# Performance work log

Hardware: AMD Instinct MI355X
Metric: run time of the kernel (lower is better)

## Reference

```python
import jax, jax.numpy as jnp
import numpy as np

N_M = 100000  # musicians
N_T = 100000  # tracks
E = 400000
D = 128


def _sage(x_src, x_dst, edge, W_l, b_l, W_r, n_dst):
    """PyG SAGEConv: lin_l(mean_{j in N(i)} x_src[j]) + lin_r(x_dst[i])."""
    src, dst = edge[0], edge[1]
    msg = x_src[src]                                   # [E, D] gather
    agg = jax.ops.segment_sum(msg, dst, num_segments=n_dst)
    cnt = jax.ops.segment_sum(jnp.ones((edge.shape[1],), x_src.dtype), dst,
                              num_segments=n_dst)
    agg = agg / jnp.maximum(cnt, 1.0)[:, None]         # mean aggregation
    return agg @ W_l.T + b_l + x_dst @ W_r.T


def setup_inputs() -> dict:
    key = jax.random.key(0)
    ks = jax.random.split(key, 7)
    scale = 0.05
    return {
        "x_m": jax.random.normal(ks[0], (N_M, D), jnp.float32),
        "x_t": jax.random.normal(ks[1], (N_T, D), jnp.float32),
        "Wl": jax.random.normal(ks[2], (3, 2, D, D), jnp.float32) * scale,
        "bl": jnp.zeros((3, 2, D), jnp.float32),
        "Wr": jax.random.normal(ks[3], (3, 2, D, D), jnp.float32) * scale,
        "edge_mt": jax.random.randint(ks[4], (2, E), 0, N_T, jnp.int32).astype(jnp.int64),
        "edge_tm": jax.random.randint(ks[5], (2, E), 0, N_M, jnp.int32).astype(jnp.int64),
    }


def reference(x_m, x_t, Wl, bl, Wr, edge_mt, edge_tm):
    # 3 HeteroConv(SAGEConv) layers; dropout=0.0 is identity.
    for layer in range(3):
        # edge type 0: musician -plays_on-> track  (dst = track)
        new_t = _sage(x_m, x_t, edge_mt, Wl[layer, 0], bl[layer, 0], Wr[layer, 0], N_T)
        # edge type 1: track -features-> musician  (dst = musician)
        new_m = _sage(x_t, x_m, edge_tm, Wl[layer, 1], bl[layer, 1], Wr[layer, 1], N_M)
        if layer < 2:
            new_m = jax.nn.relu(new_m)
            new_t = jax.nn.relu(new_t)
        x_m, x_t = new_m, new_t
    return x_m, x_t
```

## Files before the change

kernel.cpp:

```cpp
#include <hip/hip_runtime.h>
#include <hip/hip_bf16.h>

typedef __bf16 bf16_t;
typedef __attribute__((ext_vector_type(4))) __bf16 bf16x4;
typedef __attribute__((ext_vector_type(8))) __bf16 bf16x8;
typedef __attribute__((ext_vector_type(4))) float f32x4;

#define DIM 128
#define GTILE 32

__device__ __forceinline__ void gl_lds16(const void* g, void* l) {
    __builtin_amdgcn_global_load_lds(
        (const __attribute__((address_space(1))) unsigned int*)g,
        (__attribute__((address_space(3))) unsigned int*)l, 16, 0, 0);
}

__global__ void prep_count(const float* __restrict__ Wl, const float* __restrict__ Wr,
                           bf16_t* __restrict__ Wc,
                           const int* __restrict__ dA, int* __restrict__ cA,
                           const int* __restrict__ dB, int* __restrict__ cB, int E,
                           const float* __restrict__ xm, bf16_t* __restrict__ xbm, int CM,
                           const float* __restrict__ xt, bf16_t* __restrict__ xbt, int CT,
                           int PB, int CB) {
    int blk = blockIdx.x;
    if (blk < PB) {
        int idx = blk * 256 + threadIdx.x;
        if (idx >= 6 * 128 * 256) return;
        int k = idx & 255;
        int n = (idx >> 8) & 127;
        int s = idx >> 15;
        float v;
        if (k < 128) v = Wl[((size_t)s * 128 + n) * 128 + k];
        else         v = Wr[((size_t)s * 128 + n) * 128 + (k - 128)];
        Wc[idx] = (bf16_t)v;
    } else if (blk < PB + CB) {
        int i = (blk - PB) * 256 + threadIdx.x;
        if (i < E) atomicAdd(&cA[dA[i]], 1);
        else if (i < 2 * E) atomicAdd(&cB[dB[i - E]], 1);
    } else {
        int i = (blk - PB - CB) * 256 + threadIdx.x;
        const float* src; bf16_t* dst;
        if (i < CM) { src = xm; dst = xbm; }
        else if ((i -= CM) < CT) { src = xt; dst = xbt; }
        else return;
        float4 a = ((const float4*)src)[(size_t)i * 2];
        float4 b = ((const float4*)src)[(size_t)i * 2 + 1];
        bf16x8 r;
        r[0] = (bf16_t)a.x; r[1] = (bf16_t)a.y; r[2] = (bf16_t)a.z; r[3] = (bf16_t)a.w;
        r[4] = (bf16_t)b.x; r[5] = (bf16_t)b.y; r[6] = (bf16_t)b.z; r[7] = (bf16_t)b.w;
        *(bf16x8*)(dst + (size_t)i * 8) = r;
    }
}

__global__ __launch_bounds__(256) void scan_local2(
    const int* __restrict__ cntA, int* __restrict__ partA, int* __restrict__ bsumA,
    int MA, int NBA,
    const int* __restrict__ cntB, int* __restrict__ partB, int* __restrict__ bsumB,
    int MB) {
    int blk = blockIdx.x;
    const int* cnt; int* partial; int* blocksum; int M; int b;
    if (blk < NBA) { cnt = cntA; partial = partA; blocksum = bsumA; M = MA; b = blk; }
    else           { cnt = cntB; partial = partB; blocksum = bsumB; M = MB; b = blk - NBA; }
    __shared__ int sdata[256];
    int i = b * 256 + threadIdx.x;
    int v = (i < M) ? cnt[i] : 0;
    sdata[threadIdx.x] = v;
    __syncthreads();
    for (int off = 1; off < 256; off <<= 1) {
        int t = (threadIdx.x >= off) ? sdata[threadIdx.x - off] : 0;
        __syncthreads();
        sdata[threadIdx.x] += t;
        __syncthreads();
    }
    int incl = sdata[threadIdx.x];
    if (i < M) partial[i] = incl - v;
    if (threadIdx.x == 255) blocksum[b] = incl;
}

__global__ __launch_bounds__(256) void scan_blocks2(int* __restrict__ bsA, int NA,
                                                    int* __restrict__ bsB, int NBcnt) {
    int* blocksum = blockIdx.x ? bsB : bsA;
    int NB = blockIdx.x ? NBcnt : NA;
    __shared__ int sdata[256];
    __shared__ int running;
    if (threadIdx.x == 0) running = 0;
    __syncthreads();
    for (int base = 0; base < NB; base += 256) {
        int i = base + threadIdx.x;
        int v = (i < NB) ? blocksum[i] : 0;
        sdata[threadIdx.x] = v;
        __syncthreads();
        for (int off = 1; off < 256; off <<= 1) {
            int t = (threadIdx.x >= off) ? sdata[threadIdx.x - off] : 0;
            __syncthreads();
            sdata[threadIdx.x] += t;
            __syncthreads();
        }
        int incl = sdata[threadIdx.x];
        int r = running;
        __syncthreads();
        if (i < NB) blocksum[i] = incl - v + r;
        if (threadIdx.x == 0) running = r + sdata[255];
        __syncthreads();
    }
}

__global__ __launch_bounds__(256) void add_offsets2(
    const int* __restrict__ pA, const int* __restrict__ bsA,
    int* __restrict__ rsA, int* __restrict__ curA, int MA, int NBA,
    const int* __restrict__ pB, const int* __restrict__ bsB,
    int* __restrict__ rsB, int* __restrict__ curB, int MB) {
    int blk = blockIdx.x;
    const int *partial, *blocksum; int *rowstart, *cursor; int M, b;
    if (blk < NBA) { partial = pA; blocksum = bsA; rowstart = rsA; cursor = curA; M = MA; b = blk; }
    else           { partial = pB; blocksum = bsB; rowstart = rsB; cursor = curB; M = MB; b = blk - NBA; }
    int i = b * 256 + threadIdx.x;
    if (i < M) {
        int rs = partial[i] + blocksum[i >> 8];
        rowstart[i] = rs;
        cursor[i] = rs;
    }
}

__global__ void bin_edges2(const int* __restrict__ sA, const int* __restrict__ dA,
                           int* __restrict__ curA, int* __restrict__ csrA,
                           const int* __restrict__ sB, const int* __restrict__ dB,
                           int* __restrict__ curB, int* __restrict__ csrB, int E) {
    int e = blockIdx.x * blockDim.x + threadIdx.x;
    if (e < E) {
        int d = dA[e];
        int pos = atomicAdd(&curA[d], 1);
        csrA[pos] = sA[e];
    } else if (e < 2 * E) {
        int i = e - E;
        int d = dB[i];
        int pos = atomicAdd(&curB[d], 1);
        csrB[pos] = sB[i];
    }
}

#define A0SZ 8192
#define A1SZ 8192

template <int MODE>
__global__ __launch_bounds__(256, 3) void fused2(
    const bf16_t* __restrict__ gsA, const int* __restrict__ rsA,
    const int* __restrict__ cnA, const int* __restrict__ csA,
    const bf16_t* __restrict__ a1A, const bf16_t* __restrict__ WcA,
    const float* __restrict__ bA, void* __restrict__ oA, int Ma,
    const bf16_t* __restrict__ gsB, const int* __restrict__ rsB,
    const int* __restrict__ cnB, const int* __restrict__ csB,
    const bf16_t* __restrict__ a1B, const bf16_t* __restrict__ WcB,
    const float* __restrict__ bB, void* __restrict__ oB, int Mb) {
    __shared__ char smem[A0SZ + 2 * A1SZ];

    const int tid  = threadIdx.x;
    const int wid  = tid >> 6;
    const int lane = tid & 63;
    const int quad = lane >> 4;
    const int l16  = lane & 15;

    const int side = blockIdx.x & 1;
    const int t0   = blockIdx.x >> 1;
    const int gs   = gridDim.x >> 1;

    const bf16_t *gsrc, *a1p; const int *rsx, *cnx, *csx;
    const bf16_t* Wc; const float* bias; void* outp; int M;
    if (side == 0) { gsrc = gsA; rsx = rsA; cnx = cnA; csx = csA; a1p = a1A;
                     Wc = WcA; bias = bA; outp = oA; M = Ma; }
    else           { gsrc = gsB; rsx = rsB; cnx = cnB; csx = csB; a1p = a1B;
                     Wc = WcB; bias = bB; outp = oB; M = Mb; }
    const int nt = (M + GTILE - 1) / GTILE;
    if (t0 >= nt) return;

    bf16x8 breg[2][8];
#pragma unroll
    for (int ct = 0; ct < 2; ++ct)
#pragma unroll
        for (int kt = 0; kt < 8; ++kt)
            breg[ct][kt] = *(const bf16x8*)(
                Wc + (size_t)(wid * 32 + ct * 16 + l16) * 256 + kt * 32 + quad * 8);

    const float bcol0 = bias[wid * 32 + l16];
    const float bcol1 = bias[wid * 32 + 16 + l16];
    const int sw = l16 & 7;

    int s_row[2], s_off[2];
#pragma unroll
    for (int c = 0; c < 2; ++c) {
        int o = wid * 2048 + c * 1024 + lane * 16;
        int row = o >> 8;
        int ch  = (o >> 4) & 15;
        s_row[c] = row;
        s_off[c] = (ch ^ (row & 7)) * 8;
    }

    auto STAGE = [&](int b, int t) {
        const int r0 = t * GTILE;
        char* base = smem + A0SZ + b * A1SZ;
#pragma unroll
        for (int c = 0; c < 2; ++c) {
            int grow = r0 + s_row[c]; if (grow >= M) grow = M - 1;
            gl_lds16(a1p + (size_t)grow * DIM + s_off[c],
                     base + wid * 2048 + c * 1024);
        }
    };

    auto GATHER = [&](int t) {
        const int hw  = tid >> 5;
        const int l32 = tid & 31;
        char* a0 = smem;
#pragma unroll 1
        for (int rr = 0; rr < 4; ++rr) {
            int r = hw * 4 + rr;
            int d = t * GTILE + r;
            float4 acc0 = {0.f, 0.f, 0.f, 0.f};
            float4 acc1 = {0.f, 0.f, 0.f, 0.f};
            int n = 0;
            if (d < M) {
                int start = rsx[d];
                n = cnx[d];
                for (int k = 0; k < n; k += 8) {
                    int sv[8];
#pragma unroll
                    for (int j = 0; j < 8; ++j)
                        sv[j] = csx[start + min(k + j, n - 1)];
                    float4 vv[8];
#pragma unroll
                    for (int j = 0; j < 8; ++j) {
                        bf16x4 b4 = *(const bf16x4*)(gsrc + (size_t)sv[j] * DIM + l32 * 4);
                        vv[j] = (float4){(float)b4[0], (float)b4[1],
                                         (float)b4[2], (float)b4[3]};
                    }
#pragma unroll
                    for (int j = 0; j < 8; j += 2) {
                        float w0 = (k + j     < n) ? 1.f : 0.f;
                        float w1 = (k + j + 1 < n) ? 1.f : 0.f;
                        acc0.x += vv[j].x * w0; acc0.y += vv[j].y * w0;
                        acc0.z += vv[j].z * w0; acc0.w += vv[j].w * w0;
                        acc1.x += vv[j + 1].x * w1; acc1.y += vv[j + 1].y * w1;
                        acc1.z += vv[j + 1].z * w1; acc1.w += vv[j + 1].w * w1;
                    }
                }
            }
            float invn = 1.0f / (float)max(n, 1);
            bf16x4 res;
            res[0] = (bf16_t)((acc0.x + acc1.x) * invn);
            res[1] = (bf16_t)((acc0.y + acc1.y) * invn);
            res[2] = (bf16_t)((acc0.z + acc1.z) * invn);
            res[3] = (bf16_t)((acc0.w + acc1.w) * invn);
            *(bf16x4*)(a0 + r * 256 + (((l32 >> 1) ^ (r & 7)) << 4) + ((l32 & 1) << 3)) = res;
        }
    };

    auto COMPUTE = [&](int b, int t) {
        const int r0 = t * GTILE;
        const char* a0base = smem;
        const char* a1base = smem + A0SZ + b * A1SZ;
        f32x4 acc[2][2];
#pragma unroll
        for (int rt = 0; rt < 2; ++rt) {
            acc[rt][0] = (f32x4){0.f, 0.f, 0.f, 0.f};
            acc[rt][1] = (f32x4){0.f, 0.f, 0.f, 0.f};
        }
#pragma unroll
        for (int rt = 0; rt < 2; ++rt) {
            const int row = rt * 16 + l16;
            bf16x8 alo[4];
#pragma unroll
            for (int kt = 0; kt < 4; ++kt)
                alo[kt] = *(const bf16x8*)(a0base + row * 256 + ((kt * 4 + quad) ^ sw) * 16);
#pragma unroll
            for (int kt = 0; kt < 4; ++kt) {
                acc[rt][0] = __builtin_amdgcn_mfma_f32_16x16x32_bf16(alo[kt], breg[0][kt], acc[rt][0], 0, 0, 0);
                acc[rt][1] = __builtin_amdgcn_mfma_f32_16x16x32_bf16(alo[kt], breg[1][kt], acc[rt][1], 0, 0, 0);
            }
#pragma unroll
            for (int kt = 0; kt < 4; ++kt) {
                bf16x8 ah = *(const bf16x8*)(a1base + row * 256 + ((kt * 4 + quad) ^ sw) * 16);
                acc[rt][0] = __builtin_amdgcn_mfma_f32_16x16x32_bf16(ah, breg[0][kt + 4], acc[rt][0], 0, 0, 0);
                acc[rt][1] = __builtin_amdgcn_mfma_f32_16x16x32_bf16(ah, breg[1][kt + 4], acc[rt][1], 0, 0, 0);
            }
        }
#pragma unroll
        for (int ct = 0; ct < 2; ++ct) {
            const int col = wid * 32 + ct * 16 + l16;
            const float bv = ct ? bcol1 : bcol0;
#pragma unroll
            for (int rt = 0; rt < 2; ++rt)
#pragma unroll
                for (int r = 0; r < 4; ++r) {
                    int row = r0 + rt * 16 + quad * 4 + r;
                    if (row < M) {
                        float v = acc[rt][ct][r] + bv;
                        if (MODE == 1) v = fmaxf(v, 0.f);
                        if constexpr (MODE == 2)
                            ((float*)outp)[(size_t)row * DIM + col] = v;
                        else
                            ((bf16_t*)outp)[(size_t)row * DIM + col] = (bf16_t)v;
                    }
                }
        }
    };

    STAGE(0, t0);
    int cur = 0;
    for (int t = t0; t < nt; t += gs, cur ^= 1) {
        const int nxt = t + gs;
        if (nxt < nt) STAGE(cur ^ 1, nxt);
        GATHER(t);
        __syncthreads();
        COMPUTE(cur, t);
        __syncthreads();
    }
}

extern "C" void kernel_launch(void* const* d_in, const int* in_sizes, int n_in,
                              void* d_out, int out_size, void* d_ws, size_t ws_size,
                              hipStream_t stream) {
    const float* x_m = (const float*)d_in[0];
    const float* x_t = (const float*)d_in[1];
    const float* Wl  = (const float*)d_in[2];
    const float* bl  = (const float*)d_in[3];
    const float* Wr  = (const float*)d_in[4];
    const int* e_mt  = (const int*)d_in[5];
    const int* e_tm  = (const int*)d_in[6];

    const int Mm = in_sizes[0] / DIM;
    const int Mt = in_sizes[1] / DIM;
    const int E  = in_sizes[5] / 2;
    const int NBt = (Mt + 255) / 256;
    const int NBm = (Mm + 255) / 256;

    float* out_m = (float*)d_out;
    float* out_t = (float*)d_out + (size_t)Mm * DIM;

    char* ws = (char*)d_ws;
    size_t off = 0;
    auto alloc = [&](size_t bytes) -> void* {
        void* p = ws + off;
        off += (bytes + 255) & ~(size_t)255;
        return p;
    };
    bf16_t* xbm    = (bf16_t*)alloc((size_t)Mm * DIM * 2);
    bf16_t* xbt    = (bf16_t*)alloc((size_t)Mt * DIM * 2);
    bf16_t* xb_m0  = (bf16_t*)alloc((size_t)Mm * DIM * 2);
    bf16_t* xb_t0  = (bf16_t*)alloc((size_t)Mt * DIM * 2);
    bf16_t* xb_m1  = (bf16_t*)alloc((size_t)Mm * DIM * 2);
    bf16_t* xb_t1  = (bf16_t*)alloc((size_t)Mt * DIM * 2);
    int*    cnt_t  = (int*)alloc((size_t)Mt * 4);
    int*    cnt_m  = (int*)alloc((size_t)Mm * 4);
    int*    rs_t   = (int*)alloc((size_t)Mt * 4);
    int*    rs_m   = (int*)alloc((size_t)Mm * 4);
    int*    cur_tb = (int*)alloc((size_t)Mt * 4);
    int*    cur_mb = (int*)alloc((size_t)Mm * 4);
    int*    part_t = (int*)alloc((size_t)Mt * 4);
    int*    part_m = (int*)alloc((size_t)Mm * 4);
    int*    bsum_t = (int*)alloc((size_t)NBt * 4);
    int*    bsum_m = (int*)alloc((size_t)NBm * 4);
    int*    csr_t  = (int*)alloc((size_t)E * 4);
    int*    csr_m  = (int*)alloc((size_t)E * 4);
    bf16_t* Wc     = (bf16_t*)alloc((size_t)6 * 128 * 256 * 2);

    hipMemsetAsync(cnt_t, 0, (size_t)Mt * 4, stream);
    hipMemsetAsync(cnt_m, 0, (size_t)Mm * 4, stream);

    const int CM = Mm * DIM / 8, CT = Mt * DIM / 8;
    const int PB = (6 * 128 * 256 + 255) / 256;
    const int CB = (2 * E + 255) / 256;
    const int XB = (CM + CT + 255) / 256;
    prep_count<<<PB + CB + XB, 256, 0, stream>>>(Wl, Wr, Wc,
                                                 e_mt + E, cnt_t, e_tm + E, cnt_m, E,
                                                 x_m, xbm, CM, x_t, xbt, CT, PB, CB);

    scan_local2<<<NBt + NBm, 256, 0, stream>>>(cnt_t, part_t, bsum_t, Mt, NBt,
                                               cnt_m, part_m, bsum_m, Mm);
    scan_blocks2<<<2, 256, 0, stream>>>(bsum_t, NBt, bsum_m, NBm);
    add_offsets2<<<NBt + NBm, 256, 0, stream>>>(part_t, bsum_t, rs_t, cur_tb, Mt, NBt,
                                                part_m, bsum_m, rs_m, cur_mb, Mm);
    bin_edges2<<<(2 * E + 255) / 256, 256, 0, stream>>>(e_mt, e_mt + E, cur_tb, csr_t,
                                                        e_tm, e_tm + E, cur_mb, csr_m, E);

    int GG = 1536;
    {
        int ntT = (Mt + GTILE - 1) / GTILE, ntM = (Mm + GTILE - 1) / GTILE;
        int need = 2 * ((ntT > ntM) ? ntT : ntM);
        if (GG > need) GG = need;
        GG &= ~1;
        if (GG < 2) GG = 2;
    }

    const float* biasT0 = bl + 0 * DIM;  const float* biasM0 = bl + 1 * DIM;
    const float* biasT1 = bl + 2 * DIM;  const float* biasM1 = bl + 3 * DIM;
    const float* biasT2 = bl + 4 * DIM;  const float* biasM2 = bl + 5 * DIM;
    const bf16_t* WcT0 = Wc + 0 * 128 * 256;  const bf16_t* WcM0 = Wc + 1 * 128 * 256;
    const bf16_t* WcT1 = Wc + 2 * 128 * 256;  const bf16_t* WcM1 = Wc + 3 * 128 * 256;
    const bf16_t* WcT2 = Wc + 4 * 128 * 256;  const bf16_t* WcM2 = Wc + 5 * 128 * 256;

    fused2<1><<<GG, 256, 0, stream>>>(
        xbm, rs_t, cnt_t, csr_t, xbt, WcT0, biasT0, xb_t0, Mt,
        xbt, rs_m, cnt_m, csr_m, xbm, WcM0, biasM0, xb_m0, Mm);
    fused2<1><<<GG, 256, 0, stream>>>(
        xb_m0, rs_t, cnt_t, csr_t, xb_t0, WcT1, biasT1, xb_t1, Mt,
        xb_t0, rs_m, cnt_m, csr_m, xb_m0, WcM1, biasM1, xb_m1, Mm);
    fused2<2><<<GG, 256, 0, stream>>>(
        xb_m1, rs_t, cnt_t, csr_t, xb_t1, WcT2, biasT2, out_t, Mt,
        xb_t1, rs_m, cnt_m, csr_m, xb_m1, WcM2, biasM2, out_m, Mm);
}
```

Before: 527.5 us.

## Merge three-kernel scan into one wave-shuffle scan and interleave two-row gathers

Replaces the three-pass prefix scan (local scan, block-sum scan, add offsets) with a single kernel of two 1024-thread blocks. Each block walks its whole count array using wave shuffles and writes a trailing rowstart entry, so degree is now taken as rs[d+1]-rs[d] and the separate count array is no longer read in the fused layers. The neighbor-mean gather now handles two destination rows at once with 4-wide unrolled loads, keeping more independent memory requests in flight. The trade-offs are a serial scan run by only two blocks, and wasted clamped loads when the two interleaved rows have different degrees.

```diff
diff --git a/kernel.cpp b/kernel.cpp
--- a/kernel.cpp
+++ b/kernel.cpp
@@ -52,74 +52,48 @@
     }
 }
 
-__global__ __launch_bounds__(256) void scan_local2(
-    const int* __restrict__ cntA, int* __restrict__ partA, int* __restrict__ bsumA,
-    int MA, int NBA,
-    const int* __restrict__ cntB, int* __restrict__ partB, int* __restrict__ bsumB,
-    int MB) {
-    int blk = blockIdx.x;
-    const int* cnt; int* partial; int* blocksum; int M; int b;
-    if (blk < NBA) { cnt = cntA; partial = partA; blocksum = bsumA; M = MA; b = blk; }
-    else           { cnt = cntB; partial = partB; blocksum = bsumB; M = MB; b = blk - NBA; }
-    __shared__ int sdata[256];
-    int i = b * 256 + threadIdx.x;
-    int v = (i < M) ? cnt[i] : 0;
-    sdata[threadIdx.x] = v;
+__global__ __launch_bounds__(1024) void scan_all(
+    const int* __restrict__ cntA, int* __restrict__ rsA, int* __restrict__ curA, int MA,
+    const int* __restrict__ cntB, int* __restrict__ rsB, int* __restrict__ curB, int MB) {
+    const int* cnt; int* rs; int* cur; int M;
+    if (blockIdx.x == 0) { cnt = cntA; rs = rsA; cur = curA; M = MA; }
+    else                 { cnt = cntB; rs = rsB; cur = curB; M = MB; }
+    __shared__ int swv[16];
+    __shared__ int srun;
+    const int tid  = threadIdx.x;
+    const int wave = tid >> 6;
+    const int lane = tid & 63;
+    if (tid == 0) srun = 0;
     __syncthreads();
-    for (int off = 1; off < 256; off <<= 1) {
-        int t = (threadIdx.x >= off) ? sdata[threadIdx.x - off] : 0;
-        __syncthreads();
-        sdata[threadIdx.x] += t;
-        __syncthreads();
-    }
-    int incl = sdata[threadIdx.x];
-    if (i < M) partial[i] = incl - v;
-    if (threadIdx.x == 255) blocksum[b] = incl;
-}
-
-__global__ __launch_bounds__(256) void scan_blocks2(int* __restrict__ bsA, int NA,
-                                                    int* __restrict__ bsB, int NBcnt) {
-    int* blocksum = blockIdx.x ? bsB : bsA;
-    int NB = blockIdx.x ? NBcnt : NA;
-    __shared__ int sdata[256];
-    __shared__ int running;
-    if (threadIdx.x == 0) running = 0;
-    __syncthreads();
-    for (int base = 0; base < NB; base += 256) {
-        int i = base + threadIdx.x;
-        int v = (i < NB) ? blocksum[i] : 0;
-        sdata[threadIdx.x] = v;
-        __syncthreads();
-        for (int off = 1; off < 256; off <<= 1) {
-            int t = (threadIdx.x >= off) ? sdata[threadIdx.x - off] : 0;
-            __syncthreads();
-            sdata[threadIdx.x] += t;
-            __syncthreads();
-        }
-        int incl = sdata[threadIdx.x];
-        int r = running;
-        __syncthreads();
-        if (i < NB) blocksum[i] = incl - v + r;
-        if (threadIdx.x == 0) running = r + sdata[255];
-        __syncthreads();
-    }
-}
-
-__global__ __launch_bounds__(256) void add_offsets2(
-    const int* __restrict__ pA, const int* __restrict__ bsA,
-    int* __restrict__ rsA, int* __restrict__ curA, int MA, int NBA,
-    const int* __restrict__ pB, const int* __restrict__ bsB,
-    int* __restrict__ rsB, int* __restrict__ curB, int MB) {
-    int blk = blockIdx.x;
-    const int *partial, *blocksum; int *rowstart, *cursor; int M, b;
-    if (blk < NBA) { partial = pA; blocksum = bsA; rowstart = rsA; cursor = curA; M = MA; b = blk; }
-    else           { partial = pB; blocksum = bsB; rowstart = rsB; cursor = curB; M = MB; b = blk - NBA; }
-    int i = b * 256 + threadIdx.x;
-    if (i < M) {
-        int rs = partial[i] + blocksum[i >> 8];
-        rowstart[i] = rs;
-        cursor[i] = rs;
-    }
+    for (int base = 0; base < M; base += 1024) {
+        int i = base + tid;
+        int v = (i < M) ? cnt[i] : 0;
+        int x = v;
+#pragma unroll
+        for (int off = 1; off < 64; off <<= 1) {
+            int t = __shfl_up(x, off, 64);
+            if (lane >= off) x += t;
+        }
+        if (lane == 63) swv[wave] = x;
+        __syncthreads();
+        if (wave == 0) {
+            int y = (lane < 16) ? swv[lane] : 0;
+#pragma unroll
+            for (int off = 1; off < 16; off <<= 1) {
+                int t = __shfl_up(y, off, 64);
+                if (lane >= off) y += t;
+            }
+            if (lane < 16) swv[lane] = y;
+        }
+        __syncthreads();
+        int r = srun;
+        int excl = x - v + (wave ? swv[wave - 1] : 0) + r;
+        if (i < M) { rs[i] = excl; cur[i] = excl; }
+        __syncthreads();
+        if (tid == 0) srun = r + swv[15];
+        __syncthreads();
+    }
+    if (threadIdx.x == 0) rs[M] = srun;
 }
 
 __global__ void bin_edges2(const int* __restrict__ sA, const int* __restrict__ dA,
@@ -145,11 +119,11 @@
 template <int MODE>
 __global__ __launch_bounds__(256, 3) void fused2(
     const bf16_t* __restrict__ gsA, const int* __restrict__ rsA,
-    const int* __restrict__ cnA, const int* __restrict__ csA,
+    const int* __restrict__ csA,
     const bf16_t* __restrict__ a1A, const bf16_t* __restrict__ WcA,
     const float* __restrict__ bA, void* __restrict__ oA, int Ma,
     const bf16_t* __restrict__ gsB, const int* __restrict__ rsB,
-    const int* __restrict__ cnB, const int* __restrict__ csB,
+    const int* __restrict__ csB,
     const bf16_t* __restrict__ a1B, const bf16_t* __restrict__ WcB,
     const float* __restrict__ bB, void* __restrict__ oB, int Mb) {
     __shared__ char smem[A0SZ + 2 * A1SZ];
@@ -164,11 +138,11 @@
     const int t0   = blockIdx.x >> 1;
     const int gs   = gridDim.x >> 1;
 
-    const bf16_t *gsrc, *a1p; const int *rsx, *cnx, *csx;
+    const bf16_t *gsrc, *a1p; const int *rsx, *csx;
     const bf16_t* Wc; const float* bias; void* outp; int M;
-    if (side == 0) { gsrc = gsA; rsx = rsA; cnx = cnA; csx = csA; a1p = a1A;
+    if (side == 0) { gsrc = gsA; rsx = rsA; csx = csA; a1p = a1A;
                      Wc = WcA; bias = bA; outp = oA; M = Ma; }
-    else           { gsrc = gsB; rsx = rsB; cnx = cnB; csx = csB; a1p = a1B;
+    else           { gsrc = gsB; rsx = rsB; csx = csB; a1p = a1B;
                      Wc = WcB; bias = bB; outp = oB; M = Mb; }
     const int nt = (M + GTILE - 1) / GTILE;
     if (t0 >= nt) return;
@@ -210,46 +184,71 @@
         const int hw  = tid >> 5;
         const int l32 = tid & 31;
         char* a0 = smem;
-#pragma unroll 1
-        for (int rr = 0; rr < 4; ++rr) {
-            int r = hw * 4 + rr;
-            int d = t * GTILE + r;
-            float4 acc0 = {0.f, 0.f, 0.f, 0.f};
-            float4 acc1 = {0.f, 0.f, 0.f, 0.f};
-            int n = 0;
-            if (d < M) {
-                int start = rsx[d];
-                n = cnx[d];
-                for (int k = 0; k < n; k += 8) {
-                    int sv[8];
-#pragma unroll
-                    for (int j = 0; j < 8; ++j)
-                        sv[j] = csx[start + min(k + j, n - 1)];
-                    float4 vv[8];
-#pragma unroll
-                    for (int j = 0; j < 8; ++j) {
-                        bf16x4 b4 = *(const bf16x4*)(gsrc + (size_t)sv[j] * DIM + l32 * 4);
-                        vv[j] = (float4){(float)b4[0], (float)b4[1],
-                                         (float)b4[2], (float)b4[3]};
-                    }
-#pragma unroll
-                    for (int j = 0; j < 8; j += 2) {
-                        float w0 = (k + j     < n) ? 1.f : 0.f;
-                        float w1 = (k + j + 1 < n) ? 1.f : 0.f;
-                        acc0.x += vv[j].x * w0; acc0.y += vv[j].y * w0;
-                        acc0.z += vv[j].z * w0; acc0.w += vv[j].w * w0;
-                        acc1.x += vv[j + 1].x * w1; acc1.y += vv[j + 1].y * w1;
-                        acc1.z += vv[j + 1].z * w1; acc1.w += vv[j + 1].w * w1;
-                    }
+#pragma unroll
+        for (int pr = 0; pr < 2; ++pr) {
+            const int r0 = hw * 4 + pr * 2;
+            const int r1 = r0 + 1;
+            const int d0 = t * GTILE + r0;
+            const int d1 = t * GTILE + r1;
+            int s0 = 0, n0 = 0, s1 = 0, n1 = 0;
+            if (d0 < M) { s0 = rsx[d0]; n0 = rsx[d0 + 1] - s0; }
+            if (d1 < M) { s1 = rsx[d1]; n1 = rsx[d1 + 1] - s1; }
+            const int b0 = (n0 > 0) ? s0 : 0, lim0 = (n0 > 0) ? n0 - 1 : 0;
+            const int b1 = (n1 > 0) ? s1 : 0, lim1 = (n1 > 0) ? n1 - 1 : 0;
+            float4 a00 = {0.f,0.f,0.f,0.f}, a01 = {0.f,0.f,0.f,0.f};
+            float4 a10 = {0.f,0.f,0.f,0.f}, a11 = {0.f,0.f,0.f,0.f};
+            const int nmax = max(n0, n1);
+            for (int k = 0; k < nmax; k += 4) {
+                int sv0[4], sv1[4];
+#pragma unroll
+                for (int j = 0; j < 4; ++j) {
+                    sv0[j] = csx[b0 + min(k + j, lim0)];
+                    sv1[j] = csx[b1 + min(k + j, lim1)];
                 }
-            }
-            float invn = 1.0f / (float)max(n, 1);
-            bf16x4 res;
-            res[0] = (bf16_t)((acc0.x + acc1.x) * invn);
-            res[1] = (bf16_t)((acc0.y + acc1.y) * invn);
-            res[2] = (bf16_t)((acc0.z + acc1.z) * invn);
-            res[3] = (bf16_t)((acc0.w + acc1.w) * invn);
-            *(bf16x4*)(a0 + r * 256 + (((l32 >> 1) ^ (r & 7)) << 4) + ((l32 & 1) << 3)) = res;
+                bf16x4 v0[4], v1[4];
+#pragma unroll
+                for (int j = 0; j < 4; ++j)
+                    v0[j] = *(const bf16x4*)(gsrc + (size_t)sv0[j] * DIM + l32 * 4);
+#pragma unroll
+                for (int j = 0; j < 4; ++j)
+                    v1[j] = *(const bf16x4*)(gsrc + (size_t)sv1[j] * DIM + l32 * 4);
+#pragma unroll
+                for (int j = 0; j < 4; j += 2) {
+                    float w0 = (k + j     < n0) ? 1.f : 0.f;
+                    float w1 = (k + j + 1 < n0) ? 1.f : 0.f;
+                    a00.x += (float)v0[j][0] * w0;     a00.y += (float)v0[j][1] * w0;
+                    a00.z += (float)v0[j][2] * w0;     a00.w += (float)v0[j][3] * w0;
+                    a01.x += (float)v0[j + 1][0] * w1; a01.y += (float)v0[j + 1][1] * w1;
+                    a01.z += (float)v0[j + 1][2] * w1; a01.w += (float)v0[j + 1][3] * w1;
+                }
+#pragma unroll
+                for (int j = 0; j < 4; j += 2) {
+                    float w0 = (k + j     < n1) ? 1.f : 0.f;
+                    float w1 = (k + j + 1 < n1) ? 1.f : 0.f;
+                    a10.x += (float)v1[j][0] * w0;     a10.y += (float)v1[j][1] * w0;
+                    a10.z += (float)v1[j][2] * w0;     a10.w += (float)v1[j][3] * w0;
+                    a11.x += (float)v1[j + 1][0] * w1; a11.y += (float)v1[j + 1][1] * w1;
+                    a11.z += (float)v1[j + 1][2] * w1; a11.w += (float)v1[j + 1][3] * w1;
+                }
+            }
+            {
+                float invn = 1.0f / (float)max(n0, 1);
+                bf16x4 res;
+                res[0] = (bf16_t)((a00.x + a01.x) * invn);
+                res[1] = (bf16_t)((a00.y + a01.y) * invn);
+                res[2] = (bf16_t)((a00.z + a01.z) * invn);
+                res[3] = (bf16_t)((a00.w + a01.w) * invn);
+                *(bf16x4*)(a0 + r0 * 256 + (((l32 >> 1) ^ (r0 & 7)) << 4) + ((l32 & 1) << 3)) = res;
+            }
+            {
+                float invn = 1.0f / (float)max(n1, 1);
+                bf16x4 res;
+                res[0] = (bf16_t)((a10.x + a11.x) * invn);
+                res[1] = (bf16_t)((a10.y + a11.y) * invn);
+                res[2] = (bf16_t)((a10.z + a11.z) * invn);
+                res[3] = (bf16_t)((a10.w + a11.w) * invn);
+                *(bf16x4*)(a0 + r1 * 256 + (((l32 >> 1) ^ (r1 & 7)) << 4) + ((l32 & 1) << 3)) = res;
+            }
         }
     };
 
@@ -329,8 +328,6 @@
     const int Mm = in_sizes[0] / DIM;
     const int Mt = in_sizes[1] / DIM;
     const int E  = in_sizes[5] / 2;
-    const int NBt = (Mt + 255) / 256;
-    const int NBm = (Mm + 255) / 256;
 
     float* out_m = (float*)d_out;
     float* out_t = (float*)d_out + (size_t)Mm * DIM;
@@ -350,14 +347,10 @@
     bf16_t* xb_t1  = (bf16_t*)alloc((size_t)Mt * DIM * 2);
     int*    cnt_t  = (int*)alloc((size_t)Mt * 4);
     int*    cnt_m  = (int*)alloc((size_t)Mm * 4);
-    int*    rs_t   = (int*)alloc((size_t)Mt * 4);
-    int*    rs_m   = (int*)alloc((size_t)Mm * 4);
+    int*    rs_t   = (int*)alloc((size_t)(Mt + 1) * 4);
+    int*    rs_m   = (int*)alloc((size_t)(Mm + 1) * 4);
     int*    cur_tb = (int*)alloc((size_t)Mt * 4);
     int*    cur_mb = (int*)alloc((size_t)Mm * 4);
-    int*    part_t = (int*)alloc((size_t)Mt * 4);
-    int*    part_m = (int*)alloc((size_t)Mm * 4);
-    int*    bsum_t = (int*)alloc((size_t)NBt * 4);
-    int*    bsum_m = (int*)alloc((size_t)NBm * 4);
     int*    csr_t  = (int*)alloc((size_t)E * 4);
     int*    csr_m  = (int*)alloc((size_t)E * 4);
     bf16_t* Wc     = (bf16_t*)alloc((size_t)6 * 128 * 256 * 2);
@@ -373,11 +366,8 @@
                                                  e_mt + E, cnt_t, e_tm + E, cnt_m, E,
                                                  x_m, xbm, CM, x_t, xbt, CT, PB, CB);
 
-    scan_local2<<<NBt + NBm, 256, 0, stream>>>(cnt_t, part_t, bsum_t, Mt, NBt,
-                                               cnt_m, part_m, bsum_m, Mm);
-    scan_blocks2<<<2, 256, 0, stream>>>(bsum_t, NBt, bsum_m, NBm);
-    add_offsets2<<<NBt + NBm, 256, 0, stream>>>(part_t, bsum_t, rs_t, cur_tb, Mt, NBt,
-                                                part_m, bsum_m, rs_m, cur_mb, Mm);
+    scan_all<<<2, 1024, 0, stream>>>(cnt_t, rs_t, cur_tb, Mt,
+                                     cnt_m, rs_m, cur_mb, Mm);
     bin_edges2<<<(2 * E + 255) / 256, 256, 0, stream>>>(e_mt, e_mt + E, cur_tb, csr_t,
                                                         e_tm, e_tm + E, cur_mb, csr_m, E);
 
@@ -398,12 +388,12 @@
     const bf16_t* WcT2 = Wc + 4 * 128 * 256;  const bf16_t* WcM2 = Wc + 5 * 128 * 256;
 
     fused2<1><<<GG, 256, 0, stream>>>(
-        xbm, rs_t, cnt_t, csr_t, xbt, WcT0, biasT0, xb_t0, Mt,
-        xbt, rs_m, cnt_m, csr_m, xbm, WcM0, biasM0, xb_m0, Mm);
+        xbm, rs_t, csr_t, xbt, WcT0, biasT0, xb_t0, Mt,
+        xbt, rs_m, csr_m, xbm, WcM0, biasM0, xb_m0, Mm);
     fused2<1><<<GG, 256, 0, stream>>>(
-        xb_m0, rs_t, cnt_t, csr_t, xb_t0, WcT1, biasT1, xb_t1, Mt,
-        xb_t0, rs_m, cnt_m, csr_m, xb_m0, WcM1, biasM1, xb_m1, Mm);
+        xb_m0, rs_t, csr_t, xb_t0, WcT1, biasT1, xb_t1, Mt,
+        xb_t0, rs_m, csr_m, xb_m0, WcM1, biasM1, xb_m1, Mm);
     fused2<2><<<GG, 256, 0, stream>>>(
-        xb_m1, rs_t, cnt_t, csr_t, xb_t1, WcT2, biasT2, out_t, Mt,
-        xb_t1, rs_m, cnt_m, csr_m, xb_m1, WcM2, biasM2, out_m, Mm);
-}
+        xb_m1, rs_t, csr_t, xb_t1, WcT2, biasT2, out_t, Mt,
+        xb_t1, rs_m, csr_m, xb_m1, WcM2, biasM2, out_m, Mm);
+}
```

Result: slower. 594.4 us (+12.7%).
